# Kernel optimization log

Hardware: AMD Instinct MI355X
Metric: run time of the kernel (lower is better)

## Reference

```python
import jax, jax.numpy as jnp
import numpy as np

NEG_SLOPE = 0.2

def gat_layer(x, W, al, ar, src, dst, n_dst):
    # x: [Ns, Fin]; W: [Fin, H*D]; al/ar: [H, D]; src/dst: [E]
    H, D = al.shape
    h = (x @ W).reshape(-1, H, D)          # [Ns, H, D]
    h_dst = h[:n_dst]                       # dst nodes are prefix of src nodes (DGL block)
    el = (h * al).sum(-1)                   # [Ns, H]
    er = (h_dst * ar).sum(-1)               # [Nd, H]
    e = jax.nn.leaky_relu(el[src] + er[dst], NEG_SLOPE)  # [E, H]
    m = jax.ops.segment_max(e, dst, num_segments=n_dst)  # stable edge-softmax
    a = jnp.exp(e - m[dst])
    s = jax.ops.segment_sum(a, dst, num_segments=n_dst)
    alpha = a / s[dst]                      # [E, H]
    msg = h[src] * alpha[:, :, None]        # [E, H, D]
    out = jax.ops.segment_sum(msg, dst, num_segments=n_dst)  # [Nd, H, D]
    return out.reshape(n_dst, H * D)


def setup_inputs() -> dict:
    key = jax.random.key(0)
    ks = jax.random.split(key, 16)
    N0, N1, N2, N3 = 200000, 100000, 50000, 25000
    E0, E1, E2 = 1000000, 500000, 250000
    Fin, Dh, H, C = 256, 64, 3, 40
    inp = {}
    inp['x'] = jax.random.normal(ks[0], (N0, Fin), jnp.float32)
    inp['src0'] = jax.random.randint(ks[1], (E0,), 0, N0, jnp.int32)
    inp['dst0'] = jnp.sort(jax.random.randint(ks[2], (E0,), 0, N1, jnp.int32))
    inp['src1'] = jax.random.randint(ks[3], (E1,), 0, N1, jnp.int32)
    inp['dst1'] = jnp.sort(jax.random.randint(ks[4], (E1,), 0, N2, jnp.int32))
    inp['src2'] = jax.random.randint(ks[5], (E2,), 0, N2, jnp.int32)
    inp['dst2'] = jnp.sort(jax.random.randint(ks[6], (E2,), 0, N3, jnp.int32))
    sc = lambda f: np.float32(1.0 / np.sqrt(f))
    inp['W0'] = jax.random.normal(ks[7], (Fin, H * Dh), jnp.float32) * sc(Fin)
    inp['al0'] = jax.random.normal(ks[8], (H, Dh), jnp.float32) * sc(Dh)
    inp['ar0'] = jax.random.normal(ks[9], (H, Dh), jnp.float32) * sc(Dh)
    inp['W1'] = jax.random.normal(ks[10], (H * Dh, H * Dh), jnp.float32) * sc(H * Dh)
    inp['al1'] = jax.random.normal(ks[11], (H, Dh), jnp.float32) * sc(Dh)
    inp['ar1'] = jax.random.normal(ks[12], (H, Dh), jnp.float32) * sc(Dh)
    inp['W2'] = jax.random.normal(ks[13], (H * Dh, C), jnp.float32) * sc(H * Dh)
    inp['al2'] = jax.random.normal(ks[14], (1, C), jnp.float32) * sc(C)
    inp['ar2'] = jax.random.normal(ks[15], (1, C), jnp.float32) * sc(C)
    return inp


def reference(x, src0, dst0, src1, dst1, src2, dst2,
              W0, al0, ar0, W1, al1, ar1, W2, al2, ar2):
    N1, N2, N3 = 100000, 50000, 25000
    h = gat_layer(x, W0, al0, ar0, src0, dst0, N1)
    h = jax.nn.relu(h)  # dropout is identity in eval/deterministic mode
    h = gat_layer(h, W1, al1, ar1, src1, dst1, N2)
    h = jax.nn.relu(h)
    out = gat_layer(h, W2, al2, ar2, src2, dst2, N3)  # [N3, n_classes]
    return out
```

## Files before the change

kernel.cpp:

```cpp
#include <hip/hip_runtime.h>
#include <math.h>

#define DEV_INLINE __device__ __forceinline__

typedef __attribute__((ext_vector_type(8))) short short8v;
typedef __attribute__((ext_vector_type(4))) short short4v;
typedef __attribute__((ext_vector_type(4))) float float4v;

DEV_INLINE unsigned short f2bf_rtn(float f) {
  unsigned u = __float_as_uint(f);
  u += 0x7FFFu + ((u >> 16) & 1u);
  return (unsigned short)(u >> 16);
}
DEV_INLINE float bf2f(unsigned short s) { return __uint_as_float(((unsigned)s) << 16); }

DEV_INLINE int soff(int row, int oct) {
  return row * 32 + (((oct ^ (row >> 1)) & 3) << 3);
}

__global__ void conv_w_all(const float* __restrict__ W0, const float* __restrict__ W1,
                           const float* __restrict__ W2, short* __restrict__ w0h,
                           short* __restrict__ w0l, short* __restrict__ w1h,
                           short* __restrict__ w1l, short* __restrict__ w2h,
                           short* __restrict__ w2l) {
  const int S0 = 256 * 192, S1 = 192 * 192, S2 = 192 * 40;
  int idx = blockIdx.x * 256 + threadIdx.x;
  const float* W; short *Wh, *Wl; int K, N;
  if (idx < S0) { W = W0; Wh = w0h; Wl = w0l; K = 256; N = 192; }
  else if (idx < S0 + S1) { idx -= S0; W = W1; Wh = w1h; Wl = w1l; K = 192; N = 192; }
  else if (idx < S0 + S1 + S2) { idx -= S0 + S1; W = W2; Wh = w2h; Wl = w2l; K = 192; N = 40; }
  else return;
  int n = idx / K, k = idx - n * K;
  float w = W[(size_t)k * N + n];
  unsigned short h = f2bf_rtn(w);
  Wh[idx] = (short)h;
  Wl[idx] = (short)f2bf_rtn(w - bf2f(h));
}

__global__ void csr_all(const int* __restrict__ d0, const int* __restrict__ d1,
                        const int* __restrict__ d2, int* __restrict__ o0,
                        int* __restrict__ o1, int* __restrict__ o2,
                        int E0, int E1, int E2, int n1, int n2, int n3) {
  int i = blockIdx.x * 256 + threadIdx.x;
  const int* dst; int* off; int E, nd;
  if (i < E0) { dst = d0; off = o0; E = E0; nd = n1; }
  else if (i < E0 + E1) { i -= E0; dst = d1; off = o1; E = E1; nd = n2; }
  else if (i < E0 + E1 + E2) { i -= E0 + E1; dst = d2; off = o2; E = E2; nd = n3; }
  else return;
  int d = dst[i];
  int p = (i == 0) ? -1 : dst[i - 1];
  for (int q = p + 1; q <= d; ++q) off[q] = i;
  if (i == E - 1)
    for (int q = d + 1; q <= nd; ++q) off[q] = E;
}

template <int NT, int H, int ELS, bool SPLIT>
__global__ __launch_bounds__(256, 2) void gemm_fused(
    const float* __restrict__ A, const short* __restrict__ Ah,
    const short* __restrict__ Al, const short* __restrict__ Bth,
    const short* __restrict__ Btl, const float* __restrict__ al,
    const float* __restrict__ ar, float* __restrict__ C,
    float* __restrict__ el, float* __restrict__ er,
    int M, int N, int K, int n_dst) {
  constexpr int BN = NT * 16;
  constexpr int BREP = (BN + 63) / 64;
  constexpr int TPH = NT / H;
  __shared__ short As_h[128 * 32], As_l[128 * 32];
  __shared__ short Bs_h[BN * 32], Bs_l[BN * 32];
  const int tid = threadIdx.x;
  const int w = tid >> 6, lane = tid & 63;
  const int quad = lane >> 4, l16 = lane & 15;
  const int m0 = blockIdx.x * 128;

  float4v acc[2][NT];
#pragma unroll
  for (int mt = 0; mt < 2; ++mt)
#pragma unroll
    for (int nt = 0; nt < NT; ++nt)
#pragma unroll
      for (int r = 0; r < 4; ++r) acc[mt][nt][r] = 0.f;

  const int sr = tid >> 2;
  const int oct = tid & 3;

  for (int k0 = 0; k0 < K; k0 += 32) {
    short8v ah_reg[2], al_reg[2];
    float4 a0[2], a1[2];
    if (SPLIT) {
#pragma unroll
      for (int p = 0; p < 2; ++p) {
        int gr = m0 + sr + p * 64;
        if (gr < M) {
          ah_reg[p] = *(const short8v*)(Ah + (size_t)gr * K + k0 + oct * 8);
          al_reg[p] = *(const short8v*)(Al + (size_t)gr * K + k0 + oct * 8);
        } else {
#pragma unroll
          for (int j = 0; j < 8; ++j) { ah_reg[p][j] = 0; al_reg[p][j] = 0; }
        }
      }
    } else {
#pragma unroll
      for (int p = 0; p < 2; ++p) {
        int gr = m0 + sr + p * 64;
        if (gr < M) {
          const float* ap = A + (size_t)gr * K + k0 + oct * 8;
          a0[p] = *(const float4*)ap;
          a1[p] = *(const float4*)(ap + 4);
        } else {
          a0[p] = make_float4(0.f, 0.f, 0.f, 0.f);
          a1[p] = a0[p];
        }
      }
    }
    short8v bh[BREP], bl[BREP];
#pragma unroll
    for (int q = 0; q < BREP; ++q) {
      int n = sr + q * 64;
      if (n < BN) {
        if (n < N) {
          bh[q] = *(const short8v*)(Bth + (size_t)n * K + k0 + oct * 8);
          bl[q] = *(const short8v*)(Btl + (size_t)n * K + k0 + oct * 8);
        } else {
#pragma unroll
          for (int j = 0; j < 8; ++j) { bh[q][j] = 0; bl[q][j] = 0; }
        }
      }
    }
    __syncthreads();
#pragma unroll
    for (int p = 0; p < 2; ++p) {
      int r = sr + p * 64;
      short8v hv, lv;
      if (SPLIT) {
        hv = ah_reg[p];
        lv = al_reg[p];
      } else {
        float vs[8] = {a0[p].x, a0[p].y, a0[p].z, a0[p].w,
                       a1[p].x, a1[p].y, a1[p].z, a1[p].w};
#pragma unroll
        for (int j = 0; j < 8; ++j) {
          unsigned short h = f2bf_rtn(vs[j]);
          hv[j] = (short)h;
          lv[j] = (short)f2bf_rtn(vs[j] - bf2f(h));
        }
      }
      *(short8v*)(As_h + soff(r, oct)) = hv;
      *(short8v*)(As_l + soff(r, oct)) = lv;
    }
#pragma unroll
    for (int q = 0; q < BREP; ++q) {
      int n = sr + q * 64;
      if (n < BN) {
        *(short8v*)(Bs_h + soff(n, oct)) = bh[q];
        *(short8v*)(Bs_l + soff(n, oct)) = bl[q];
      }
    }
    __syncthreads();
    short8v afh[2], afl[2];
#pragma unroll
    for (int mt = 0; mt < 2; ++mt) {
      int row = w * 32 + mt * 16 + l16;
      afh[mt] = *(const short8v*)(As_h + soff(row, quad));
      afl[mt] = *(const short8v*)(As_l + soff(row, quad));
    }
#pragma unroll
    for (int nt = 0; nt < NT; ++nt) {
      int col = nt * 16 + l16;
      short8v bfh = *(const short8v*)(Bs_h + soff(col, quad));
      short8v bfl = *(const short8v*)(Bs_l + soff(col, quad));
#pragma unroll
      for (int mt = 0; mt < 2; ++mt) {
        acc[mt][nt] = __builtin_amdgcn_mfma_f32_16x16x32_bf16(afh[mt], bfh, acc[mt][nt], 0, 0, 0);
        acc[mt][nt] = __builtin_amdgcn_mfma_f32_16x16x32_bf16(afh[mt], bfl, acc[mt][nt], 0, 0, 0);
        acc[mt][nt] = __builtin_amdgcn_mfma_f32_16x16x32_bf16(afl[mt], bfh, acc[mt][nt], 0, 0, 0);
      }
    }
  }

  float av[NT], rv[NT];
#pragma unroll
  for (int nt = 0; nt < NT; ++nt) {
    int col = nt * 16 + l16;
    av[nt] = (col < N) ? al[col] : 0.f;
    rv[nt] = (col < N) ? ar[col] : 0.f;
  }
#pragma unroll
  for (int mt = 0; mt < 2; ++mt)
#pragma unroll
    for (int r = 0; r < 4; ++r) {
      int gm = m0 + w * 32 + mt * 16 + quad * 4 + r;
      if (gm >= M) continue;
      float pl[H], pr[H];
#pragma unroll
      for (int h = 0; h < H; ++h) { pl[h] = 0.f; pr[h] = 0.f; }
#pragma unroll
      for (int nt = 0; nt < NT; ++nt) {
        int h = nt / TPH;
        pl[h] = fmaf(acc[mt][nt][r], av[nt], pl[h]);
        pr[h] = fmaf(acc[mt][nt][r], rv[nt], pr[h]);
      }
#pragma unroll
      for (int h = 0; h < H; ++h) {
#pragma unroll
        for (int o = 8; o >= 1; o >>= 1) {
          pl[h] += __shfl_xor(pl[h], o, 16);
          pr[h] += __shfl_xor(pr[h], o, 16);
        }
      }
      if (l16 == 0) {
#pragma unroll
        for (int h = 0; h < H; ++h) {
          el[(size_t)gm * ELS + h] = pl[h];
          if (gm < n_dst) er[(size_t)gm * ELS + h] = pr[h];
        }
      }
#pragma unroll
      for (int nt = 0; nt < NT; ++nt) {
        int col = nt * 16 + l16;
        if (col < N) C[(size_t)gm * N + col] = acc[mt][nt][r];
      }
    }
}

template <int H, int D, int ELS, bool RELU, bool SPLIT_OUT>
__global__ __launch_bounds__(256) void agg3_kernel(
    const float* __restrict__ hsrc, const float* __restrict__ el,
    const float* __restrict__ er, const int* __restrict__ src,
    const int* __restrict__ off, float* __restrict__ outf,
    short* __restrict__ outh, short* __restrict__ outl, int n_dst) {
  constexpr int F = H * D;
  constexpr int NP = (F + 63) / 64;
  __shared__ float wbuf[16][16][H];
  __shared__ int sbuf[16][16];
  const int g = threadIdx.x >> 4, l = threadIdx.x & 15;
  const int d = blockIdx.x * 16 + g;
  if (d >= n_dst) return;
  const int lo = off[d], hi = off[d + 1];

  if (hi <= lo) {
#pragma unroll
    for (int p = 0; p < NP; ++p) {
      int c4 = (p * 16 + l) * 4;
      if (c4 < F) {
        if (SPLIT_OUT) {
          short4v z;
#pragma unroll
          for (int j = 0; j < 4; ++j) z[j] = 0;
          *(short4v*)(outh + (size_t)d * F + c4) = z;
          *(short4v*)(outl + (size_t)d * F + c4) = z;
        } else {
          *(float4*)(outf + (size_t)d * F + c4) = make_float4(0.f, 0.f, 0.f, 0.f);
        }
      }
    }
    return;
  }

  float erv[H], s_part[H];
  if (H == 3) {
    float4 t = *(const float4*)(er + (size_t)d * ELS);
    erv[0] = t.x;
    if (H > 1) { erv[1] = t.y; erv[2] = t.z; }
  } else {
    erv[0] = er[(size_t)d * ELS];
  }
#pragma unroll
  for (int h = 0; h < H; ++h) s_part[h] = 0.f;
  float4 acc[NP];
#pragma unroll
  for (int p = 0; p < NP; ++p) acc[p] = make_float4(0.f, 0.f, 0.f, 0.f);

  for (int base = lo; base < hi; base += 16) {
    const int i = base + l;
    const bool valid = i < hi;
    const int sid = valid ? src[i] : 0;
    sbuf[g][l] = sid;
    float evs[H];
    if (H == 3) {
      float4 t = valid ? *(const float4*)(el + (size_t)sid * ELS)
                       : make_float4(0.f, 0.f, 0.f, 0.f);
      evs[0] = t.x;
      if (H > 1) { evs[1] = t.y; evs[2] = t.z; }
    } else {
      evs[0] = valid ? el[(size_t)sid * ELS] : 0.f;
    }
#pragma unroll
    for (int h = 0; h < H; ++h) {
      float e = 0.f;
      if (valid) {
        e = evs[h] + erv[h];
        e = e > 0.f ? e : 0.2f * e;
        e = __expf(e);
      }
      s_part[h] += e;
      wbuf[g][l][h] = e;
    }

    const int cnt = min(16, hi - base);
    float4 h0[NP], h1[NP], h2[NP];
    const int sj0 = sbuf[g][0];
    const int sj1 = sbuf[g][cnt > 1 ? 1 : 0];
#pragma unroll
    for (int p = 0; p < NP; ++p) {
      int c4 = (p * 16 + l) * 4;
      if (c4 < F) {
        h0[p] = *(const float4*)(hsrc + (size_t)sj0 * F + c4);
        h1[p] = *(const float4*)(hsrc + (size_t)sj1 * F + c4);
      } else {
        h0[p] = make_float4(0.f, 0.f, 0.f, 0.f);
        h1[p] = h0[p];
      }
    }
    for (int ei = 0; ei < cnt; ++ei) {
      if (ei + 2 < cnt) {
        const int sj2 = sbuf[g][ei + 2];
#pragma unroll
        for (int p = 0; p < NP; ++p) {
          int c4 = (p * 16 + l) * 4;
          h2[p] = (c4 < F) ? *(const float4*)(hsrc + (size_t)sj2 * F + c4)
                           : make_float4(0.f, 0.f, 0.f, 0.f);
        }
      }
#pragma unroll
      for (int p = 0; p < NP; ++p) {
        int c4 = (p * 16 + l) * 4;
        float wc = wbuf[g][ei][c4 / D];
        acc[p].x = fmaf(wc, h0[p].x, acc[p].x);
        acc[p].y = fmaf(wc, h0[p].y, acc[p].y);
        acc[p].z = fmaf(wc, h0[p].z, acc[p].z);
        acc[p].w = fmaf(wc, h0[p].w, acc[p].w);
      }
#pragma unroll
      for (int p = 0; p < NP; ++p) { h0[p] = h1[p]; h1[p] = h2[p]; }
    }
  }

#pragma unroll
  for (int h = 0; h < H; ++h)
#pragma unroll
    for (int o = 8; o >= 1; o >>= 1) s_part[h] += __shfl_xor(s_part[h], o, 16);

#pragma unroll
  for (int p = 0; p < NP; ++p) {
    int c4 = (p * 16 + l) * 4;
    if (c4 < F) {
      float inv = 1.f / s_part[c4 / D];
      float4 o;
      o.x = acc[p].x * inv; o.y = acc[p].y * inv;
      o.z = acc[p].z * inv; o.w = acc[p].w * inv;
      if (RELU) {
        o.x = fmaxf(o.x, 0.f); o.y = fmaxf(o.y, 0.f);
        o.z = fmaxf(o.z, 0.f); o.w = fmaxf(o.w, 0.f);
      }
      if (SPLIT_OUT) {
        float vs[4] = {o.x, o.y, o.z, o.w};
        short4v sh, sl;
#pragma unroll
        for (int j = 0; j < 4; ++j) {
          unsigned short hh = f2bf_rtn(vs[j]);
          sh[j] = (short)hh;
          sl[j] = (short)f2bf_rtn(vs[j] - bf2f(hh));
        }
        *(short4v*)(outh + (size_t)d * F + c4) = sh;
        *(short4v*)(outl + (size_t)d * F + c4) = sl;
      } else {
        *(float4*)(outf + (size_t)d * F + c4) = o;
      }
    }
  }
}

extern "C" void kernel_launch(void* const* d_in, const int* in_sizes, int n_in,
                              void* d_out, int out_size, void* d_ws, size_t ws_size,
                              hipStream_t stream) {
  const float* x   = (const float*)d_in[0];
  const int* src0  = (const int*)d_in[1];
  const int* dst0  = (const int*)d_in[2];
  const int* src1  = (const int*)d_in[3];
  const int* dst1  = (const int*)d_in[4];
  const int* src2  = (const int*)d_in[5];
  const int* dst2  = (const int*)d_in[6];
  const float* W0  = (const float*)d_in[7];
  const float* al0 = (const float*)d_in[8];
  const float* ar0 = (const float*)d_in[9];
  const float* W1  = (const float*)d_in[10];
  const float* al1 = (const float*)d_in[11];
  const float* ar1 = (const float*)d_in[12];
  const float* W2  = (const float*)d_in[13];
  const float* al2 = (const float*)d_in[14];
  const float* ar2 = (const float*)d_in[15];

  const int N0 = 200000, N1 = 100000, N2 = 50000, N3 = 25000;
  const int E0 = in_sizes[1], E1 = in_sizes[3], E2 = in_sizes[5];
  const int Fin = 256, F = 192, C = 40;

  float* ws     = (float*)d_ws;
  float* h_buf  = ws;
  float* el_buf = h_buf + (size_t)N0 * F;
  float* er_buf = el_buf + (size_t)N0 * 4;
  short* o_hi   = (short*)(er_buf + (size_t)N1 * 4);
  short* o_lo   = o_hi + (size_t)N1 * F;
  short* w0h    = o_lo + (size_t)N1 * F;
  short* w0l    = w0h + 192 * 256;
  short* w1h    = w0l + 192 * 256;
  short* w1l    = w1h + 192 * 192;
  short* w2h    = w1l + 192 * 192;
  short* w2l    = w2h + 40 * 192;
  int*   off0   = (int*)(w2l + 40 * 192);
  int*   off1   = off0 + (N1 + 1);
  int*   off2   = off1 + (N2 + 1);

  dim3 blk(256);

  const int WTOT = 256 * 192 + 192 * 192 + 192 * 40;
  conv_w_all<<<dim3((WTOT + 255) / 256), blk, 0, stream>>>(W0, W1, W2, w0h, w0l, w1h, w1l, w2h, w2l);
  const int ETOT = E0 + E1 + E2;
  csr_all<<<dim3((ETOT + 255) / 256), blk, 0, stream>>>(dst0, dst1, dst2, off0, off1, off2,
                                                        E0, E1, E2, N1, N2, N3);

  gemm_fused<12, 3, 4, false><<<dim3((N0 + 127) / 128), blk, 0, stream>>>(
      x, nullptr, nullptr, w0h, w0l, al0, ar0, h_buf, el_buf, er_buf, N0, F, Fin, N1);
  agg3_kernel<3, 64, 4, true, true><<<dim3((N1 + 15) / 16), blk, 0, stream>>>(
      h_buf, el_buf, er_buf, src0, off0, nullptr, o_hi, o_lo, N1);

  gemm_fused<12, 3, 4, true><<<dim3((N1 + 127) / 128), blk, 0, stream>>>(
      nullptr, o_hi, o_lo, w1h, w1l, al1, ar1, h_buf, el_buf, er_buf, N1, F, F, N2);
  agg3_kernel<3, 64, 4, true, true><<<dim3((N2 + 15) / 16), blk, 0, stream>>>(
      h_buf, el_buf, er_buf, src1, off1, nullptr, o_hi, o_lo, N2);

  gemm_fused<3, 1, 1, true><<<dim3((N2 + 127) / 128), blk, 0, stream>>>(
      nullptr, o_hi, o_lo, w2h, w2l, al2, ar2, h_buf, el_buf, er_buf, N2, C, F, N3);
  agg3_kernel<1, 40, 1, false, false><<<dim3((N3 + 15) / 16), blk, 0, stream>>>(
      h_buf, el_buf, er_buf, src2, off2, (float*)d_out, nullptr, nullptr, N3);
}
```

Measured before the change: 644.7 us.

## Drop LDS staging in GEMM; pre-pack weights into MFMA fragment order

Weights are pre-packed at conversion time into per-fragment MFMA order, so each lane loads its B operand straight from global memory (L2-resident). The A operand is likewise loaded directly into registers per lane, removing shared-memory tiles and both __syncthreads per K step. Block tile shrinks from 128 to 64 rows with one M-tile per wave, trading A reuse across N tiles in LDS for less sync and LDS traffic, at the cost of more redundant global/L2 B reads and uncoalesced per-lane A loads.

```diff
diff --git a/kernel.cpp b/kernel.cpp
--- a/kernel.cpp
+++ b/kernel.cpp
@@ -13,25 +13,25 @@
   return (unsigned short)(u >> 16);
 }
 DEV_INLINE float bf2f(unsigned short s) { return __uint_as_float(((unsigned)s) << 16); }
-
-DEV_INLINE int soff(int row, int oct) {
-  return row * 32 + (((oct ^ (row >> 1)) & 3) << 3);
-}
 
 __global__ void conv_w_all(const float* __restrict__ W0, const float* __restrict__ W1,
                            const float* __restrict__ W2, short* __restrict__ w0h,
                            short* __restrict__ w0l, short* __restrict__ w1h,
                            short* __restrict__ w1l, short* __restrict__ w2h,
                            short* __restrict__ w2l) {
-  const int S0 = 256 * 192, S1 = 192 * 192, S2 = 192 * 40;
+  const int S0 = 192 * 256, S1 = 192 * 192, S2 = 48 * 192;
   int idx = blockIdx.x * 256 + threadIdx.x;
-  const float* W; short *Wh, *Wl; int K, N;
-  if (idx < S0) { W = W0; Wh = w0h; Wl = w0l; K = 256; N = 192; }
-  else if (idx < S0 + S1) { idx -= S0; W = W1; Wh = w1h; Wl = w1l; K = 192; N = 192; }
-  else if (idx < S0 + S1 + S2) { idx -= S0 + S1; W = W2; Wh = w2h; Wl = w2l; K = 192; N = 40; }
+  const float* W; short *Wh, *Wl; int KS, N;
+  if (idx < S0) { W = W0; Wh = w0h; Wl = w0l; KS = 8; N = 192; }
+  else if (idx < S0 + S1) { idx -= S0; W = W1; Wh = w1h; Wl = w1l; KS = 6; N = 192; }
+  else if (idx < S0 + S1 + S2) { idx -= S0 + S1; W = W2; Wh = w2h; Wl = w2l; KS = 6; N = 40; }
   else return;
-  int n = idx / K, k = idx - n * K;
-  float w = W[(size_t)k * N + n];
+  int j = idx & 7, l16 = (idx >> 3) & 15;
+  int rem = idx >> 7;
+  int quad = rem & 3; rem >>= 2;
+  int s = rem % KS, nt = rem / KS;
+  int n = nt * 16 + l16, k = s * 32 + quad * 8 + j;
+  float w = (n < N) ? W[(size_t)k * N + n] : 0.f;
   unsigned short h = f2bf_rtn(w);
   Wh[idx] = (short)h;
   Wl[idx] = (short)f2bf_rtn(w - bf2f(h));
@@ -55,125 +55,58 @@
 }
 
 template <int NT, int H, int ELS, bool SPLIT>
-__global__ __launch_bounds__(256, 2) void gemm_fused(
+__global__ __launch_bounds__(256) void gemm_direct(
     const float* __restrict__ A, const short* __restrict__ Ah,
-    const short* __restrict__ Al, const short* __restrict__ Bth,
-    const short* __restrict__ Btl, const float* __restrict__ al,
+    const short* __restrict__ Al, const short* __restrict__ BPh,
+    const short* __restrict__ BPl, const float* __restrict__ al,
     const float* __restrict__ ar, float* __restrict__ C,
     float* __restrict__ el, float* __restrict__ er,
     int M, int N, int K, int n_dst) {
-  constexpr int BN = NT * 16;
-  constexpr int BREP = (BN + 63) / 64;
   constexpr int TPH = NT / H;
-  __shared__ short As_h[128 * 32], As_l[128 * 32];
-  __shared__ short Bs_h[BN * 32], Bs_l[BN * 32];
   const int tid = threadIdx.x;
   const int w = tid >> 6, lane = tid & 63;
   const int quad = lane >> 4, l16 = lane & 15;
-  const int m0 = blockIdx.x * 128;
-
-  float4v acc[2][NT];
-#pragma unroll
-  for (int mt = 0; mt < 2; ++mt)
-#pragma unroll
-    for (int nt = 0; nt < NT; ++nt)
-#pragma unroll
-      for (int r = 0; r < 4; ++r) acc[mt][nt][r] = 0.f;
-
-  const int sr = tid >> 2;
-  const int oct = tid & 3;
-
-  for (int k0 = 0; k0 < K; k0 += 32) {
-    short8v ah_reg[2], al_reg[2];
-    float4 a0[2], a1[2];
+  const int m0 = blockIdx.x * 64;
+  int gr = m0 + w * 16 + l16;
+  if (gr >= M) gr = M - 1;
+  const int KS = K >> 5;
+  const int fo = quad * 128 + l16 * 8;
+
+  float4v acc[NT];
+#pragma unroll
+  for (int nt = 0; nt < NT; ++nt)
+#pragma unroll
+    for (int r = 0; r < 4; ++r) acc[nt][r] = 0.f;
+
+  const size_t arow = (size_t)gr * K;
+
+#pragma unroll 2
+  for (int s = 0; s < KS; ++s) {
+    const int kq = s * 32 + quad * 8;
+    short8v afh, afl;
     if (SPLIT) {
-#pragma unroll
-      for (int p = 0; p < 2; ++p) {
-        int gr = m0 + sr + p * 64;
-        if (gr < M) {
-          ah_reg[p] = *(const short8v*)(Ah + (size_t)gr * K + k0 + oct * 8);
-          al_reg[p] = *(const short8v*)(Al + (size_t)gr * K + k0 + oct * 8);
-        } else {
-#pragma unroll
-          for (int j = 0; j < 8; ++j) { ah_reg[p][j] = 0; al_reg[p][j] = 0; }
-        }
-      }
+      afh = *(const short8v*)(Ah + arow + kq);
+      afl = *(const short8v*)(Al + arow + kq);
     } else {
-#pragma unroll
-      for (int p = 0; p < 2; ++p) {
-        int gr = m0 + sr + p * 64;
-        if (gr < M) {
-          const float* ap = A + (size_t)gr * K + k0 + oct * 8;
-          a0[p] = *(const float4*)ap;
-          a1[p] = *(const float4*)(ap + 4);
-        } else {
-          a0[p] = make_float4(0.f, 0.f, 0.f, 0.f);
-          a1[p] = a0[p];
-        }
-      }
-    }
-    short8v bh[BREP], bl[BREP];
-#pragma unroll
-    for (int q = 0; q < BREP; ++q) {
-      int n = sr + q * 64;
-      if (n < BN) {
-        if (n < N) {
-          bh[q] = *(const short8v*)(Bth + (size_t)n * K + k0 + oct * 8);
-          bl[q] = *(const short8v*)(Btl + (size_t)n * K + k0 + oct * 8);
-        } else {
-#pragma unroll
-          for (int j = 0; j < 8; ++j) { bh[q][j] = 0; bl[q][j] = 0; }
-        }
-      }
-    }
-    __syncthreads();
-#pragma unroll
-    for (int p = 0; p < 2; ++p) {
-      int r = sr + p * 64;
-      short8v hv, lv;
-      if (SPLIT) {
-        hv = ah_reg[p];
-        lv = al_reg[p];
-      } else {
-        float vs[8] = {a0[p].x, a0[p].y, a0[p].z, a0[p].w,
-                       a1[p].x, a1[p].y, a1[p].z, a1[p].w};
-#pragma unroll
-        for (int j = 0; j < 8; ++j) {
-          unsigned short h = f2bf_rtn(vs[j]);
-          hv[j] = (short)h;
-          lv[j] = (short)f2bf_rtn(vs[j] - bf2f(h));
-        }
-      }
-      *(short8v*)(As_h + soff(r, oct)) = hv;
-      *(short8v*)(As_l + soff(r, oct)) = lv;
-    }
-#pragma unroll
-    for (int q = 0; q < BREP; ++q) {
-      int n = sr + q * 64;
-      if (n < BN) {
-        *(short8v*)(Bs_h + soff(n, oct)) = bh[q];
-        *(short8v*)(Bs_l + soff(n, oct)) = bl[q];
-      }
-    }
-    __syncthreads();
-    short8v afh[2], afl[2];
-#pragma unroll
-    for (int mt = 0; mt < 2; ++mt) {
-      int row = w * 32 + mt * 16 + l16;
-      afh[mt] = *(const short8v*)(As_h + soff(row, quad));
-      afl[mt] = *(const short8v*)(As_l + soff(row, quad));
-    }
+      float4 a0 = *(const float4*)(A + arow + kq);
+      float4 a1 = *(const float4*)(A + arow + kq + 4);
+      float vs[8] = {a0.x, a0.y, a0.z, a0.w, a1.x, a1.y, a1.z, a1.w};
+#pragma unroll
+      for (int j = 0; j < 8; ++j) {
+        unsigned short h = f2bf_rtn(vs[j]);
+        afh[j] = (short)h;
+        afl[j] = (short)f2bf_rtn(vs[j] - bf2f(h));
+      }
+    }
+    const short* bh = BPh + (size_t)s * 512 + fo;
+    const short* bl = BPl + (size_t)s * 512 + fo;
 #pragma unroll
     for (int nt = 0; nt < NT; ++nt) {
-      int col = nt * 16 + l16;
-      short8v bfh = *(const short8v*)(Bs_h + soff(col, quad));
-      short8v bfl = *(const short8v*)(Bs_l + soff(col, quad));
-#pragma unroll
-      for (int mt = 0; mt < 2; ++mt) {
-        acc[mt][nt] = __builtin_amdgcn_mfma_f32_16x16x32_bf16(afh[mt], bfh, acc[mt][nt], 0, 0, 0);
-        acc[mt][nt] = __builtin_amdgcn_mfma_f32_16x16x32_bf16(afh[mt], bfl, acc[mt][nt], 0, 0, 0);
-        acc[mt][nt] = __builtin_amdgcn_mfma_f32_16x16x32_bf16(afl[mt], bfh, acc[mt][nt], 0, 0, 0);
-      }
+      short8v bfh = *(const short8v*)(bh + (size_t)nt * KS * 512);
+      short8v bfl = *(const short8v*)(bl + (size_t)nt * KS * 512);
+      acc[nt] = __builtin_amdgcn_mfma_f32_16x16x32_bf16(afh, bfh, acc[nt], 0, 0, 0);
+      acc[nt] = __builtin_amdgcn_mfma_f32_16x16x32_bf16(afh, bfl, acc[nt], 0, 0, 0);
+      acc[nt] = __builtin_amdgcn_mfma_f32_16x16x32_bf16(afl, bfh, acc[nt], 0, 0, 0);
     }
   }
 
@@ -185,41 +118,39 @@
     rv[nt] = (col < N) ? ar[col] : 0.f;
   }
 #pragma unroll
-  for (int mt = 0; mt < 2; ++mt)
-#pragma unroll
-    for (int r = 0; r < 4; ++r) {
-      int gm = m0 + w * 32 + mt * 16 + quad * 4 + r;
-      if (gm >= M) continue;
-      float pl[H], pr[H];
-#pragma unroll
-      for (int h = 0; h < H; ++h) { pl[h] = 0.f; pr[h] = 0.f; }
-#pragma unroll
-      for (int nt = 0; nt < NT; ++nt) {
-        int h = nt / TPH;
-        pl[h] = fmaf(acc[mt][nt][r], av[nt], pl[h]);
-        pr[h] = fmaf(acc[mt][nt][r], rv[nt], pr[h]);
-      }
+  for (int r = 0; r < 4; ++r) {
+    int gm = m0 + w * 16 + quad * 4 + r;
+    if (gm >= M) continue;
+    float pl[H], pr[H];
+#pragma unroll
+    for (int h = 0; h < H; ++h) { pl[h] = 0.f; pr[h] = 0.f; }
+#pragma unroll
+    for (int nt = 0; nt < NT; ++nt) {
+      int h = nt / TPH;
+      pl[h] = fmaf(acc[nt][r], av[nt], pl[h]);
+      pr[h] = fmaf(acc[nt][r], rv[nt], pr[h]);
+    }
+#pragma unroll
+    for (int h = 0; h < H; ++h) {
+#pragma unroll
+      for (int o = 8; o >= 1; o >>= 1) {
+        pl[h] += __shfl_xor(pl[h], o, 16);
+        pr[h] += __shfl_xor(pr[h], o, 16);
+      }
+    }
+    if (l16 == 0) {
 #pragma unroll
       for (int h = 0; h < H; ++h) {
-#pragma unroll
-        for (int o = 8; o >= 1; o >>= 1) {
-          pl[h] += __shfl_xor(pl[h], o, 16);
-          pr[h] += __shfl_xor(pr[h], o, 16);
-        }
-      }
-      if (l16 == 0) {
-#pragma unroll
-        for (int h = 0; h < H; ++h) {
-          el[(size_t)gm * ELS + h] = pl[h];
-          if (gm < n_dst) er[(size_t)gm * ELS + h] = pr[h];
-        }
-      }
-#pragma unroll
-      for (int nt = 0; nt < NT; ++nt) {
-        int col = nt * 16 + l16;
-        if (col < N) C[(size_t)gm * N + col] = acc[mt][nt][r];
-      }
-    }
+        el[(size_t)gm * ELS + h] = pl[h];
+        if (gm < n_dst) er[(size_t)gm * ELS + h] = pr[h];
+      }
+    }
+#pragma unroll
+    for (int nt = 0; nt < NT; ++nt) {
+      int col = nt * 16 + l16;
+      if (col < N) C[(size_t)gm * N + col] = acc[nt][r];
+    }
+  }
 }
 
 template <int H, int D, int ELS, bool RELU, bool SPLIT_OUT>
@@ -405,30 +336,30 @@
   short* w1h    = w0l + 192 * 256;
   short* w1l    = w1h + 192 * 192;
   short* w2h    = w1l + 192 * 192;
-  short* w2l    = w2h + 40 * 192;
-  int*   off0   = (int*)(w2l + 40 * 192);
+  short* w2l    = w2h + 48 * 192;
+  int*   off0   = (int*)(w2l + 48 * 192);
   int*   off1   = off0 + (N1 + 1);
   int*   off2   = off1 + (N2 + 1);
 
   dim3 blk(256);
 
-  const int WTOT = 256 * 192 + 192 * 192 + 192 * 40;
+  const int WTOT = 192 * 256 + 192 * 192 + 48 * 192;
   conv_w_all<<<dim3((WTOT + 255) / 256), blk, 0, stream>>>(W0, W1, W2, w0h, w0l, w1h, w1l, w2h, w2l);
   const int ETOT = E0 + E1 + E2;
   csr_all<<<dim3((ETOT + 255) / 256), blk, 0, stream>>>(dst0, dst1, dst2, off0, off1, off2,
                                                         E0, E1, E2, N1, N2, N3);
 
-  gemm_fused<12, 3, 4, false><<<dim3((N0 + 127) / 128), blk, 0, stream>>>(
+  gemm_direct<12, 3, 4, false><<<dim3((N0 + 63) / 64), blk, 0, stream>>>(
       x, nullptr, nullptr, w0h, w0l, al0, ar0, h_buf, el_buf, er_buf, N0, F, Fin, N1);
   agg3_kernel<3, 64, 4, true, true><<<dim3((N1 + 15) / 16), blk, 0, stream>>>(
       h_buf, el_buf, er_buf, src0, off0, nullptr, o_hi, o_lo, N1);
 
-  gemm_fused<12, 3, 4, true><<<dim3((N1 + 127) / 128), blk, 0, stream>>>(
+  gemm_direct<12, 3, 4, true><<<dim3((N1 + 63) / 64), blk, 0, stream>>>(
       nullptr, o_hi, o_lo, w1h, w1l, al1, ar1, h_buf, el_buf, er_buf, N1, F, F, N2);
   agg3_kernel<3, 64, 4, true, true><<<dim3((N2 + 15) / 16), blk, 0, stream>>>(
       h_buf, el_buf, er_buf, src1, off1, nullptr, o_hi, o_lo, N2);
 
-  gemm_fused<3, 1, 1, true><<<dim3((N2 + 127) / 128), blk, 0, stream>>>(
+  gemm_direct<3, 1, 1, true><<<dim3((N2 + 63) / 64), blk, 0, stream>>>(
       nullptr, o_hi, o_lo, w2h, w2l, al2, ar2, h_buf, el_buf, er_buf, N2, C, F, N3);
   agg3_kernel<1, 40, 1, false, false><<<dim3((N3 + 15) / 16), blk, 0, stream>>>(
       h_buf, el_buf, er_buf, src2, off2, (float*)d_out, nullptr, nullptr, N3);
```

After: 790.5 us. 1.23x slower.
